# Performance work log

Measured on AMD Instinct MI355X. Metric: run time of the kernel, lower is better.

## Reference

```python
import jax, jax.numpy as jnp
import numpy as np

B, S, D_MODEL, N_HEADS, D_K, D_V = 4, 1024, 1024, 16, 64, 64
LN_EPS = 1e-5


def setup_inputs() -> dict:
    key = jax.random.key(0)
    ks = jax.random.split(key, 10)
    inp = {
        "input_Q": jax.random.normal(ks[0], (B, S, D_MODEL), dtype=jnp.float32),
        "input_K": jax.random.normal(ks[1], (B, S, D_MODEL), dtype=jnp.float32),
        "input_V": jax.random.normal(ks[2], (B, S, D_MODEL), dtype=jnp.float32),
        "attn_mask": jax.random.randint(ks[3], (B, S, S), 0, 2) > 0,
        "res_att": jax.random.normal(ks[4], (B, N_HEADS, S, S), dtype=jnp.float32),
        # weights stored as [in, out] (torch Linear applies x @ W.T)
        "W_Q": jax.random.normal(ks[5], (D_MODEL, N_HEADS * D_K), dtype=jnp.float32) * 0.02,
        "W_K": jax.random.normal(ks[6], (D_MODEL, N_HEADS * D_K), dtype=jnp.float32) * 0.02,
        "W_V": jax.random.normal(ks[7], (D_MODEL, N_HEADS * D_V), dtype=jnp.float32) * 0.02,
        "W_fc": jax.random.normal(ks[8], (N_HEADS * D_V, D_MODEL), dtype=jnp.float32) * 0.02,
        "ln_gamma": jnp.ones((D_MODEL,), dtype=jnp.float32),
        "ln_beta": jnp.zeros((D_MODEL,), dtype=jnp.float32),
    }
    return inp


def layer_norm(x, gamma, beta):
    mu = jnp.mean(x, axis=-1, keepdims=True)
    var = jnp.mean((x - mu) ** 2, axis=-1, keepdims=True)
    return (x - mu) * jax.lax.rsqrt(var + LN_EPS) * gamma + beta


def reference(input_Q, input_K, input_V, attn_mask, res_att,
              W_Q, W_K, W_V, W_fc, ln_gamma, ln_beta):
    b, s, _ = input_Q.shape
    residual = input_Q
    # project and split heads: [B, H, S, d]
    Q = (input_Q @ W_Q).reshape(b, s, N_HEADS, D_K).transpose(0, 2, 1, 3)
    K = (input_K @ W_K).reshape(b, -1, N_HEADS, D_K).transpose(0, 2, 1, 3)
    V = (input_V @ W_V).reshape(b, -1, N_HEADS, D_V).transpose(0, 2, 1, 3)
    # scores [B, H, Sq, Sk] + residual attention bias
    scores = jnp.einsum("bhqd,bhkd->bhqk", Q, K) / np.sqrt(D_K).astype(np.float32)
    scores = scores + res_att
    scores = jnp.where(attn_mask[:, None, :, :], jnp.float32(-1e9), scores)
    attn = jax.nn.softmax(scores, axis=-1)
    context = jnp.einsum("bhqk,bhkd->bhqd", attn, V)
    context = context.transpose(0, 2, 1, 3).reshape(b, s, N_HEADS * D_V)
    output = context @ W_fc
    out = layer_norm(output + residual, ln_gamma, ln_beta)
    return (out, attn)
```

## Files before the change

### kernel.cpp

```cpp
#include <hip/hip_runtime.h>
#include <hip/hip_fp16.h>


typedef short short8 __attribute__((ext_vector_type(8)));
typedef unsigned short ushort8 __attribute__((ext_vector_type(8)));
typedef float f32x4 __attribute__((ext_vector_type(4)));
typedef int i32x4 __attribute__((ext_vector_type(4)));

__device__ __forceinline__ unsigned short f2bf(float f) {
  unsigned int u = __float_as_uint(f);
  u += 0x7fffu + ((u >> 16) & 1u);
  return (unsigned short)(u >> 16);
}

#define BAR() do { asm volatile("s_waitcnt lgkmcnt(0)" ::: "memory"); \
                   __builtin_amdgcn_s_barrier(); } while (0)

__global__ __launch_bounds__(256) void cvt3_kernel(
    const float* __restrict__ a, const float* __restrict__ b, const float* __restrict__ c,
    unsigned short* __restrict__ oa, unsigned short* __restrict__ ob, unsigned short* __restrict__ oc)
{
  const float* src = blockIdx.y == 0 ? a : (blockIdx.y == 1 ? b : c);
  unsigned short* dst = blockIdx.y == 0 ? oa : (blockIdx.y == 1 ? ob : oc);
  size_t i = (size_t)blockIdx.x * 256 + threadIdx.x;
  float4 v = ((const float4*)src)[i];
  ushort4 o;
  o.x = f2bf(v.x); o.y = f2bf(v.y); o.z = f2bf(v.z); o.w = f2bf(v.w);
  ((ushort4*)dst)[i] = o;
}

__global__ void wtrans_kernel(
    const float* __restrict__ w0, const float* __restrict__ w1,
    const float* __restrict__ w2, const float* __restrict__ w3,
    unsigned short* __restrict__ o0, unsigned short* __restrict__ o1,
    unsigned short* __restrict__ o2, unsigned short* __restrict__ o3)
{
  __shared__ float tile[32][33];
  int z = blockIdx.z;
  const float* src = z == 0 ? w0 : (z == 1 ? w1 : (z == 2 ? w2 : w3));
  unsigned short* dst = z == 0 ? o0 : (z == 1 ? o1 : (z == 2 ? o2 : o3));
  int bx = blockIdx.x * 32;
  int by = blockIdx.y * 32;
  int tx = threadIdx.x, ty = threadIdx.y;
#pragma unroll
  for (int i = 0; i < 4; ++i)
    tile[ty + 8 * i][tx] = src[(size_t)(by + ty + 8 * i) * 1024 + bx + tx];
  __syncthreads();
#pragma unroll
  for (int i = 0; i < 4; ++i)
    dst[(size_t)(bx + ty + 8 * i) * 1024 + by + tx] = f2bf(tile[tx][ty + 8 * i]);
}

__device__ __forceinline__ void gemm_core(const unsigned short* __restrict__ A,
                                          const unsigned short* __restrict__ Bt,
                                          int m0, int n0, f32x4 (&acc)[4][4])
{
  __shared__ unsigned short As[128][40];
  __shared__ unsigned short Bs[128][40];
  const int tid = threadIdx.x;
  const int lane = tid & 63;
  const int w = tid >> 6;
  const int wm = (w >> 1) << 6;
  const int wn = (w & 1) << 6;
  const int lr = lane & 15;
  const int lk = (lane >> 4) << 3;

  f32x4 zero = {0.f, 0.f, 0.f, 0.f};
#pragma unroll
  for (int mi = 0; mi < 4; ++mi)
#pragma unroll
    for (int ni = 0; ni < 4; ++ni) acc[mi][ni] = zero;

  for (int kt = 0; kt < 1024; kt += 32) {
    __syncthreads();
#pragma unroll
    for (int i = 0; i < 2; ++i) {
      int c = tid + (i << 8);
      int r = c >> 2, ko = (c & 3) << 3;
      *(short8*)&As[r][ko] = *(const short8*)&A[(size_t)(m0 + r) * 1024 + kt + ko];
      *(short8*)&Bs[r][ko] = *(const short8*)&Bt[(size_t)(n0 + r) * 1024 + kt + ko];
    }
    __syncthreads();
    short8 a[4], b[4];
#pragma unroll
    for (int mi = 0; mi < 4; ++mi) a[mi] = *(const short8*)&As[wm + mi * 16 + lr][lk];
#pragma unroll
    for (int ni = 0; ni < 4; ++ni) b[ni] = *(const short8*)&Bs[wn + ni * 16 + lr][lk];
#pragma unroll
    for (int mi = 0; mi < 4; ++mi)
#pragma unroll
      for (int ni = 0; ni < 4; ++ni)
        acc[mi][ni] = __builtin_amdgcn_mfma_f32_16x16x32_bf16(a[mi], b[ni], acc[mi][ni], 0, 0, 0);
  }
}

__global__ __launch_bounds__(256) void proj_gemm(
    const unsigned short* __restrict__ Xq, const unsigned short* __restrict__ Xk,
    const unsigned short* __restrict__ Xv,
    const unsigned short* __restrict__ Wtq, const unsigned short* __restrict__ Wtk,
    const unsigned short* __restrict__ Wtv,
    unsigned short* __restrict__ Qp, unsigned short* __restrict__ Kp,
    unsigned short* __restrict__ Vpt)
{
  const int mode = blockIdx.z;
  const unsigned short* A = mode == 0 ? Xq : (mode == 1 ? Xk : Xv);
  const unsigned short* Bt = mode == 0 ? Wtq : (mode == 1 ? Wtk : Wtv);
  const int m0 = blockIdx.y * 128;
  const int n0 = blockIdx.x * 128;

  f32x4 acc[4][4];
  gemm_core(A, Bt, m0, n0, acc);

  const int lane = threadIdx.x & 63;
  const int w = threadIdx.x >> 6;
  const int wm = (w >> 1) << 6;
  const int wn = (w & 1) << 6;
  const int lr = lane & 15;
  const int lg = lane >> 4;
  const float scale = (mode == 0) ? 0.125f : 1.0f;
  unsigned short* dst01 = (mode == 0) ? Qp : Kp;

#pragma unroll
  for (int mi = 0; mi < 4; ++mi)
#pragma unroll
    for (int ni = 0; ni < 4; ++ni)
#pragma unroll
      for (int r = 0; r < 4; ++r) {
        int m = m0 + wm + mi * 16 + (lg << 2) + r;
        int n = n0 + wn + ni * 16 + lr;
        float v = acc[mi][ni][r] * scale;
        int bb = m >> 10, ss = m & 1023, hh = n >> 6, dd = n & 63;
        if (mode < 2)
          dst01[((((size_t)bb * 16 + hh) << 10) + ss) * 64 + dd] = f2bf(v);
        else
          Vpt[((((size_t)bb * 16 + hh) * 64 + dd) << 10) + ss] = f2bf(v);
      }
}

__global__ __launch_bounds__(256) void fc_gemm(
    const unsigned short* __restrict__ Ctx, const unsigned short* __restrict__ Wtf,
    float* __restrict__ OutLin)
{
  const int m0 = blockIdx.y * 128;
  const int n0 = blockIdx.x * 128;
  f32x4 acc[4][4];
  gemm_core(Ctx, Wtf, m0, n0, acc);

  const int lane = threadIdx.x & 63;
  const int w = threadIdx.x >> 6;
  const int wm = (w >> 1) << 6;
  const int wn = (w & 1) << 6;
  const int lr = lane & 15;
  const int lg = lane >> 4;
#pragma unroll
  for (int mi = 0; mi < 4; ++mi)
#pragma unroll
    for (int ni = 0; ni < 4; ++ni)
#pragma unroll
      for (int r = 0; r < 4; ++r) {
        int m = m0 + wm + mi * 16 + (lg << 2) + r;
        int n = n0 + wn + ni * 16 + lr;
        OutLin[(size_t)m * 1024 + n] = acc[mi][ni][r];
      }
}

__global__ __launch_bounds__(256) void attn_kernel(
    const unsigned short* __restrict__ Qp, const unsigned short* __restrict__ Kp,
    const unsigned short* __restrict__ Vpt,
    const float* __restrict__ res_att, const int* __restrict__ mask,
    float* __restrict__ attn_out, unsigned short* __restrict__ Ctx)
{
  __shared__ unsigned short S16[16 * 1024];
  const int qb = blockIdx.x, h = blockIdx.y, b = blockIdx.z;
  const int q0 = qb * 16;
  const int tid = threadIdx.x;
  const int lane = tid & 63;
  const int w = tid >> 6;
  const int lr = lane & 15;
  const int lg = lane >> 4;
  const int lk = lg << 3;

  const unsigned short* Qbh = Qp + (((size_t)b * 16 + h) << 16);
  const unsigned short* Kbh = Kp + (((size_t)b * 16 + h) << 16);
  const unsigned short* Vbh = Vpt + (((size_t)b * 16 + h) << 16);
  const float* res_row = res_att + ((((size_t)b * 16 + h) * 1024 + q0) << 10);
  const int* msk_row = mask + ((((size_t)b) * 1024 + q0) << 10);
  float* attn_row = attn_out + ((((size_t)b * 16 + h) * 1024 + q0) << 10);

  short8 aq0 = *(const short8*)&Qbh[(size_t)(q0 + lr) * 64 + lk];
  short8 aq1 = *(const short8*)&Qbh[(size_t)(q0 + lr) * 64 + 32 + lk];

  f32x4 zero = {0.f, 0.f, 0.f, 0.f};
#pragma unroll 2
  for (int t = 0; t < 16; ++t) {
    int n0 = (w * 16 + t) * 16;
    short8 bk0 = *(const short8*)&Kbh[(size_t)(n0 + lr) * 64 + lk];
    short8 bk1 = *(const short8*)&Kbh[(size_t)(n0 + lr) * 64 + 32 + lk];
    int col = n0 + lr;
    float rr0 = __builtin_nontemporal_load(&res_row[((size_t)(lg * 4 + 0) << 10) + col]);
    float rr1 = __builtin_nontemporal_load(&res_row[((size_t)(lg * 4 + 1) << 10) + col]);
    float rr2 = __builtin_nontemporal_load(&res_row[((size_t)(lg * 4 + 2) << 10) + col]);
    float rr3 = __builtin_nontemporal_load(&res_row[((size_t)(lg * 4 + 3) << 10) + col]);
    int mm0 = msk_row[((size_t)(lg * 4 + 0) << 10) + col];
    int mm1 = msk_row[((size_t)(lg * 4 + 1) << 10) + col];
    int mm2 = msk_row[((size_t)(lg * 4 + 2) << 10) + col];
    int mm3 = msk_row[((size_t)(lg * 4 + 3) << 10) + col];
    f32x4 acc = zero;
    acc = __builtin_amdgcn_mfma_f32_16x16x32_bf16(aq0, bk0, acc, 0, 0, 0);
    acc = __builtin_amdgcn_mfma_f32_16x16x32_bf16(aq1, bk1, acc, 0, 0, 0);
    float s0 = mm0 ? -30000.f : acc[0] + rr0;
    float s1 = mm1 ? -30000.f : acc[1] + rr1;
    float s2 = mm2 ? -30000.f : acc[2] + rr2;
    float s3 = mm3 ? -30000.f : acc[3] + rr3;
    int cbase = (((col >> 3) ^ ((lg * 4) & 7)) << 3) | (col & 7);
#pragma unroll
    for (int r = 0; r < 4; ++r) {
      int row = lg * 4 + r;
      int idx = row * 1024 + ((((col >> 3) ^ (row & 7)) << 3) | (col & 7));
      float sv = (r == 0) ? s0 : (r == 1) ? s1 : (r == 2) ? s2 : s3;
      S16[idx] = __half_as_ushort(__float2half(sv));
    }
    (void)cbase;
  }

  BAR();

#pragma unroll
  for (int j = 0; j < 4; ++j) {
    const int r_ = w + 4 * j;
    const int swz_ = r_ & 7;
    ushort8 hv0 = *(const ushort8*)&S16[r_ * 1024 + ((lane ^ swz_) << 3)];
    ushort8 hv1 = *(const ushort8*)&S16[r_ * 1024 + (((64 + lane) ^ swz_) << 3)];
    float sv[16];
#pragma unroll
    for (int e = 0; e < 8; ++e) {
      sv[e]     = __expf(__half2float(__ushort_as_half(hv0[e])));
      sv[8 + e] = __expf(__half2float(__ushort_as_half(hv1[e])));
    }
    float s01 = sv[0] + sv[1], s23 = sv[2] + sv[3];
    float s45 = sv[4] + sv[5], s67 = sv[6] + sv[7];
    float s89 = sv[8] + sv[9], sab = sv[10] + sv[11];
    float scd = sv[12] + sv[13], sef = sv[14] + sv[15];
    float sum = ((s01 + s23) + (s45 + s67)) + ((s89 + sab) + (scd + sef));
#pragma unroll
    for (int off = 32; off >= 1; off >>= 1) sum += __shfl_xor(sum, off);
    float inv = 1.f / sum;
#pragma unroll
    for (int i = 0; i < 16; ++i) sv[i] *= inv;
    f32x4* att4 = (f32x4*)(attn_row + ((size_t)r_ << 10));
    f32x4 o0 = {sv[0], sv[1], sv[2], sv[3]};
    f32x4 o1 = {sv[4], sv[5], sv[6], sv[7]};
    f32x4 o2 = {sv[8], sv[9], sv[10], sv[11]};
    f32x4 o3 = {sv[12], sv[13], sv[14], sv[15]};
    att4[lane * 2] = o0;
    att4[lane * 2 + 1] = o1;
    att4[128 + lane * 2] = o2;
    att4[128 + lane * 2 + 1] = o3;
    ushort8 q0_, q1_;
#pragma unroll
    for (int e = 0; e < 8; ++e) { q0_[e] = f2bf(sv[e]); q1_[e] = f2bf(sv[8 + e]); }
    *(ushort8*)&S16[r_ * 1024 + ((lane ^ swz_) << 3)] = q0_;
    *(ushort8*)&S16[r_ * 1024 + (((64 + lane) ^ swz_) << 3)] = q1_;
  }

  BAR();

  f32x4 co = zero;
  const int dv0 = w * 16;
  const int pswz = lr & 7;
#pragma unroll 4
  for (int ks = 0; ks < 32; ++ks) {
    int u = (ks << 2) + lg;
    short8 pa = *(const short8*)&S16[lr * 1024 + ((u ^ pswz) << 3)];
    short8 bv = *(const short8*)&Vbh[(size_t)(dv0 + lr) * 1024 + (ks << 5) + lk];
    co = __builtin_amdgcn_mfma_f32_16x16x32_bf16(pa, bv, co, 0, 0, 0);
  }
#pragma unroll
  for (int r = 0; r < 4; ++r) {
    int row = (lg << 2) + r;
    Ctx[((size_t)(b * 1024 + q0 + row)) * 1024 + h * 64 + dv0 + lr] = f2bf(co[r]);
  }
}

__global__ __launch_bounds__(256) void ln_kernel(
    const float* __restrict__ xlin, const float* __restrict__ resid,
    const float* __restrict__ gamma, const float* __restrict__ beta,
    float* __restrict__ out)
{
  const int m = blockIdx.x;
  const int t = threadIdx.x;
  float4 v = ((const float4*)(xlin + ((size_t)m << 10)))[t];
  float4 rq = ((const float4*)(resid + ((size_t)m << 10)))[t];
  v.x += rq.x; v.y += rq.y; v.z += rq.z; v.w += rq.w;
  float s = v.x + v.y + v.z + v.w;
  float s2 = v.x * v.x + v.y * v.y + v.z * v.z + v.w * v.w;
#pragma unroll
  for (int off = 32; off >= 1; off >>= 1) {
    s += __shfl_xor(s, off);
    s2 += __shfl_xor(s2, off);
  }
  __shared__ float rs[4], rs2[4];
  const int w = t >> 6, lane = t & 63;
  if (lane == 0) { rs[w] = s; rs2[w] = s2; }
  __syncthreads();
  s = rs[0] + rs[1] + rs[2] + rs[3];
  s2 = rs2[0] + rs2[1] + rs2[2] + rs2[3];
  float mu = s * (1.f / 1024.f);
  float var = s2 * (1.f / 1024.f) - mu * mu;
  float rstd = rsqrtf(var + 1e-5f);
  float4 g = ((const float4*)gamma)[t];
  float4 bt = ((const float4*)beta)[t];
  float4 o;
  o.x = (v.x - mu) * rstd * g.x + bt.x;
  o.y = (v.y - mu) * rstd * g.y + bt.y;
  o.z = (v.z - mu) * rstd * g.z + bt.z;
  o.w = (v.w - mu) * rstd * g.w + bt.w;
  ((float4*)(out + ((size_t)m << 10)))[t] = o;
}

extern "C" void kernel_launch(void* const* d_in, const int* in_sizes, int n_in,
                              void* d_out, int out_size, void* d_ws, size_t ws_size,
                              hipStream_t stream) {
  const float* inQ = (const float*)d_in[0];
  const float* inK = (const float*)d_in[1];
  const float* inV = (const float*)d_in[2];
  const int* msk = (const int*)d_in[3];
  const float* res = (const float*)d_in[4];
  const float* wq = (const float*)d_in[5];
  const float* wk = (const float*)d_in[6];
  const float* wv = (const float*)d_in[7];
  const float* wfc = (const float*)d_in[8];
  const float* gamma = (const float*)d_in[9];
  const float* beta = (const float*)d_in[10];

  unsigned short* Xq = (unsigned short*)d_ws;
  unsigned short* Xk = Xq + 4194304;
  unsigned short* Xv = Xk + 4194304;
  unsigned short* Wtq = Xv + 4194304;
  unsigned short* Wtk = Wtq + 1048576;
  unsigned short* Wtv = Wtk + 1048576;
  unsigned short* Wtf = Wtv + 1048576;
  unsigned short* Qp = Wtf + 1048576;
  unsigned short* Kp = Qp + 4194304;
  unsigned short* Vpt = Kp + 4194304;
  unsigned short* Ctx = Vpt + 4194304;
  float* OutLin = (float*)d_ws;

  float* out = (float*)d_out;
  float* attn_out = out + 4194304;

  cvt3_kernel<<<dim3(4096, 3, 1), 256, 0, stream>>>(inQ, inK, inV, Xq, Xk, Xv);
  wtrans_kernel<<<dim3(32, 32, 4), dim3(32, 8, 1), 0, stream>>>(wq, wk, wv, wfc, Wtq, Wtk, Wtv, Wtf);
  proj_gemm<<<dim3(8, 32, 3), 256, 0, stream>>>(Xq, Xk, Xv, Wtq, Wtk, Wtv, Qp, Kp, Vpt);
  attn_kernel<<<dim3(64, 16, 4), 256, 0, stream>>>(Qp, Kp, Vpt, res, msk, attn_out, Ctx);
  fc_gemm<<<dim3(8, 32, 1), 256, 0, stream>>>(Ctx, Wtf, OutLin);
  ln_kernel<<<dim3(4096, 1, 1), 256, 0, stream>>>(OutLin, inQ, gamma, beta, out);
}
```

Before: 319.6 us.

## Compute exp in score pass, defer softmax normalization to attn write and PV output

The score loop now applies exp directly and accumulates per-row partial sums in registers, reducing them across lanes and waves through a small shared array. Unnormalized exp values are stored as bf16 in LDS and used unnormalized for the PV matmul, with the 1/sum scaling applied to the context output instead. This removes the second LDS write pass, one barrier, and the per-row wave reductions. In exchange, attn values are now derived from bf16-rounded exponentials rather than fp16 scores, there is no max subtraction so exp can overflow on large scores, and masked entries become exact zeros.

Result: slower. 339.1 us (+6.1%).

```diff
diff --git a/kernel.cpp b/kernel.cpp
--- a/kernel.cpp
+++ b/kernel.cpp
@@ -11,6 +11,9 @@
   unsigned int u = __float_as_uint(f);
   u += 0x7fffu + ((u >> 16) & 1u);
   return (unsigned short)(u >> 16);
+}
+__device__ __forceinline__ float bf2f(unsigned short u) {
+  return __uint_as_float(((unsigned int)u) << 16);
 }
 
 #define BAR() do { asm volatile("s_waitcnt lgkmcnt(0)" ::: "memory"); \
@@ -171,6 +174,7 @@
     float* __restrict__ attn_out, unsigned short* __restrict__ Ctx)
 {
   __shared__ unsigned short S16[16 * 1024];
+  __shared__ float part[4][4][4];
   const int qb = blockIdx.x, h = blockIdx.y, b = blockIdx.z;
   const int q0 = qb * 16;
   const int tid = threadIdx.x;
@@ -191,6 +195,7 @@
   short8 aq1 = *(const short8*)&Qbh[(size_t)(q0 + lr) * 64 + 32 + lk];
 
   f32x4 zero = {0.f, 0.f, 0.f, 0.f};
+  float psum0 = 0.f, psum1 = 0.f, psum2 = 0.f, psum3 = 0.f;
 #pragma unroll 2
   for (int t = 0; t < 16; ++t) {
     int n0 = (w * 16 + t) * 16;
@@ -208,19 +213,33 @@
     f32x4 acc = zero;
     acc = __builtin_amdgcn_mfma_f32_16x16x32_bf16(aq0, bk0, acc, 0, 0, 0);
     acc = __builtin_amdgcn_mfma_f32_16x16x32_bf16(aq1, bk1, acc, 0, 0, 0);
-    float s0 = mm0 ? -30000.f : acc[0] + rr0;
-    float s1 = mm1 ? -30000.f : acc[1] + rr1;
-    float s2 = mm2 ? -30000.f : acc[2] + rr2;
-    float s3 = mm3 ? -30000.f : acc[3] + rr3;
-    int cbase = (((col >> 3) ^ ((lg * 4) & 7)) << 3) | (col & 7);
+    float e0 = mm0 ? 0.f : __expf(acc[0] + rr0);
+    float e1 = mm1 ? 0.f : __expf(acc[1] + rr1);
+    float e2 = mm2 ? 0.f : __expf(acc[2] + rr2);
+    float e3 = mm3 ? 0.f : __expf(acc[3] + rr3);
+    psum0 += e0; psum1 += e1; psum2 += e2; psum3 += e3;
+    int cs = ((((col >> 3)) << 3) | (col & 7));
 #pragma unroll
     for (int r = 0; r < 4; ++r) {
       int row = lg * 4 + r;
       int idx = row * 1024 + ((((col >> 3) ^ (row & 7)) << 3) | (col & 7));
-      float sv = (r == 0) ? s0 : (r == 1) ? s1 : (r == 2) ? s2 : s3;
-      S16[idx] = __half_as_ushort(__float2half(sv));
+      float ev = (r == 0) ? e0 : (r == 1) ? e1 : (r == 2) ? e2 : e3;
+      S16[idx] = f2bf(ev);
     }
-    (void)cbase;
+    (void)cs;
+  }
+#pragma unroll
+  for (int off = 1; off <= 8; off <<= 1) {
+    psum0 += __shfl_xor(psum0, off);
+    psum1 += __shfl_xor(psum1, off);
+    psum2 += __shfl_xor(psum2, off);
+    psum3 += __shfl_xor(psum3, off);
+  }
+  if (lr == 0) {
+    part[w][lg][0] = psum0;
+    part[w][lg][1] = psum1;
+    part[w][lg][2] = psum2;
+    part[w][lg][3] = psum3;
   }
 
   BAR();
@@ -229,41 +248,25 @@
   for (int j = 0; j < 4; ++j) {
     const int r_ = w + 4 * j;
     const int swz_ = r_ & 7;
+    const int lgr = r_ >> 2, rr_ = r_ & 3;
+    float sum = part[0][lgr][rr_] + part[1][lgr][rr_] + part[2][lgr][rr_] + part[3][lgr][rr_];
+    float inv = 1.f / sum;
     ushort8 hv0 = *(const ushort8*)&S16[r_ * 1024 + ((lane ^ swz_) << 3)];
     ushort8 hv1 = *(const ushort8*)&S16[r_ * 1024 + (((64 + lane) ^ swz_) << 3)];
-    float sv[16];
-#pragma unroll
-    for (int e = 0; e < 8; ++e) {
-      sv[e]     = __expf(__half2float(__ushort_as_half(hv0[e])));
-      sv[8 + e] = __expf(__half2float(__ushort_as_half(hv1[e])));
+    f32x4 o0, o1, o2, o3;
+#pragma unroll
+    for (int e = 0; e < 4; ++e) {
+      o0[e] = bf2f(hv0[e]) * inv;
+      o1[e] = bf2f(hv0[4 + e]) * inv;
+      o2[e] = bf2f(hv1[e]) * inv;
+      o3[e] = bf2f(hv1[4 + e]) * inv;
     }
-    float s01 = sv[0] + sv[1], s23 = sv[2] + sv[3];
-    float s45 = sv[4] + sv[5], s67 = sv[6] + sv[7];
-    float s89 = sv[8] + sv[9], sab = sv[10] + sv[11];
-    float scd = sv[12] + sv[13], sef = sv[14] + sv[15];
-    float sum = ((s01 + s23) + (s45 + s67)) + ((s89 + sab) + (scd + sef));
-#pragma unroll
-    for (int off = 32; off >= 1; off >>= 1) sum += __shfl_xor(sum, off);
-    float inv = 1.f / sum;
-#pragma unroll
-    for (int i = 0; i < 16; ++i) sv[i] *= inv;
     f32x4* att4 = (f32x4*)(attn_row + ((size_t)r_ << 10));
-    f32x4 o0 = {sv[0], sv[1], sv[2], sv[3]};
-    f32x4 o1 = {sv[4], sv[5], sv[6], sv[7]};
-    f32x4 o2 = {sv[8], sv[9], sv[10], sv[11]};
-    f32x4 o3 = {sv[12], sv[13], sv[14], sv[15]};
     att4[lane * 2] = o0;
     att4[lane * 2 + 1] = o1;
     att4[128 + lane * 2] = o2;
     att4[128 + lane * 2 + 1] = o3;
-    ushort8 q0_, q1_;
-#pragma unroll
-    for (int e = 0; e < 8; ++e) { q0_[e] = f2bf(sv[e]); q1_[e] = f2bf(sv[8 + e]); }
-    *(ushort8*)&S16[r_ * 1024 + ((lane ^ swz_) << 3)] = q0_;
-    *(ushort8*)&S16[r_ * 1024 + (((64 + lane) ^ swz_) << 3)] = q1_;
-  }
-
-  BAR();
+  }
 
   f32x4 co = zero;
   const int dv0 = w * 16;
@@ -278,7 +281,9 @@
 #pragma unroll
   for (int r = 0; r < 4; ++r) {
     int row = (lg << 2) + r;
-    Ctx[((size_t)(b * 1024 + q0 + row)) * 1024 + h * 64 + dv0 + lr] = f2bf(co[r]);
+    float sum = part[0][lg][r] + part[1][lg][r] + part[2][lg][r] + part[3][lg][r];
+    float inv = 1.f / sum;
+    Ctx[((size_t)(b * 1024 + q0 + row)) * 1024 + h * 64 + dv0 + lr] = f2bf(co[r] * inv);
   }
 }
 
```

## Split attention into QK-exp kernel and PV-normalize kernel via bf16 scratch

Applied to the files above, without the earlier changes.

Replaces the single fused attention kernel with two kernels. The first computes QK scores, adds the residual bias, applies the mask and exp, writes unnormalized bf16 exponentials to a 128MB workspace, and stores per-wave partial row sums. The second reads those exponentials to write the normalized fp32 attention and to run the PV MFMA product. The intent is to remove the LDS staging and barrier of the fused kernel and raise occupancy, at the cost of an extra large global round trip for the exponentials. It also drops the max subtraction, so exp can overflow if scores are large, and falls back to the fused kernel when the workspace is too small.

Result: slower. 479.2 us (+49.9%).

```diff
diff --git a/kernel.cpp b/kernel.cpp
--- a/kernel.cpp
+++ b/kernel.cpp
@@ -11,6 +11,9 @@
   unsigned int u = __float_as_uint(f);
   u += 0x7fffu + ((u >> 16) & 1u);
   return (unsigned short)(u >> 16);
+}
+__device__ __forceinline__ float bf2f(unsigned short u) {
+  return __uint_as_float(((unsigned int)u) << 16);
 }
 
 #define BAR() do { asm volatile("s_waitcnt lgkmcnt(0)" ::: "memory"); \
@@ -164,7 +167,138 @@
       }
 }
 
-__global__ __launch_bounds__(256) void attn_kernel(
+
+__global__ __launch_bounds__(256) void qk_exp_kernel(
+    const unsigned short* __restrict__ Qp, const unsigned short* __restrict__ Kp,
+    const float* __restrict__ res_att, const int* __restrict__ mask,
+    unsigned short* __restrict__ E, float* __restrict__ psum_ws)
+{
+  const int qb = blockIdx.x, h = blockIdx.y, b = blockIdx.z;
+  const int bh = b * 16 + h;
+  const int q0 = qb * 16;
+  const int tid = threadIdx.x;
+  const int lane = tid & 63;
+  const int w = tid >> 6;
+  const int lr = lane & 15;
+  const int lg = lane >> 4;
+  const int lk = lg << 3;
+
+  const unsigned short* Qbh = Qp + ((size_t)bh << 16);
+  const unsigned short* Kbh = Kp + ((size_t)bh << 16);
+  const float* res_row = res_att + (((size_t)bh * 1024 + q0) << 10);
+  const int* msk_row = mask + ((((size_t)b) * 1024 + q0) << 10);
+  unsigned short* e_row = E + (((size_t)bh * 1024 + q0) << 10);
+
+  short8 aq0 = *(const short8*)&Qbh[(size_t)(q0 + lr) * 64 + lk];
+  short8 aq1 = *(const short8*)&Qbh[(size_t)(q0 + lr) * 64 + 32 + lk];
+
+  f32x4 zero = {0.f, 0.f, 0.f, 0.f};
+  float psum0 = 0.f, psum1 = 0.f, psum2 = 0.f, psum3 = 0.f;
+#pragma unroll 2
+  for (int t = 0; t < 16; ++t) {
+    int n0 = (w * 16 + t) * 16;
+    short8 bk0 = *(const short8*)&Kbh[(size_t)(n0 + lr) * 64 + lk];
+    short8 bk1 = *(const short8*)&Kbh[(size_t)(n0 + lr) * 64 + 32 + lk];
+    int col = n0 + lr;
+    float rr0 = __builtin_nontemporal_load(&res_row[((size_t)(lg * 4 + 0) << 10) + col]);
+    float rr1 = __builtin_nontemporal_load(&res_row[((size_t)(lg * 4 + 1) << 10) + col]);
+    float rr2 = __builtin_nontemporal_load(&res_row[((size_t)(lg * 4 + 2) << 10) + col]);
+    float rr3 = __builtin_nontemporal_load(&res_row[((size_t)(lg * 4 + 3) << 10) + col]);
+    int mm0 = msk_row[((size_t)(lg * 4 + 0) << 10) + col];
+    int mm1 = msk_row[((size_t)(lg * 4 + 1) << 10) + col];
+    int mm2 = msk_row[((size_t)(lg * 4 + 2) << 10) + col];
+    int mm3 = msk_row[((size_t)(lg * 4 + 3) << 10) + col];
+    f32x4 acc = zero;
+    acc = __builtin_amdgcn_mfma_f32_16x16x32_bf16(aq0, bk0, acc, 0, 0, 0);
+    acc = __builtin_amdgcn_mfma_f32_16x16x32_bf16(aq1, bk1, acc, 0, 0, 0);
+    float e0 = mm0 ? 0.f : __expf(acc[0] + rr0);
+    float e1 = mm1 ? 0.f : __expf(acc[1] + rr1);
+    float e2 = mm2 ? 0.f : __expf(acc[2] + rr2);
+    float e3 = mm3 ? 0.f : __expf(acc[3] + rr3);
+    psum0 += e0; psum1 += e1; psum2 += e2; psum3 += e3;
+    e_row[((size_t)(lg * 4 + 0) << 10) + col] = f2bf(e0);
+    e_row[((size_t)(lg * 4 + 1) << 10) + col] = f2bf(e1);
+    e_row[((size_t)(lg * 4 + 2) << 10) + col] = f2bf(e2);
+    e_row[((size_t)(lg * 4 + 3) << 10) + col] = f2bf(e3);
+  }
+#pragma unroll
+  for (int off = 1; off <= 8; off <<= 1) {
+    psum0 += __shfl_xor(psum0, off);
+    psum1 += __shfl_xor(psum1, off);
+    psum2 += __shfl_xor(psum2, off);
+    psum3 += __shfl_xor(psum3, off);
+  }
+  if (lr == 0) {
+    size_t base = ((size_t)bh * 1024 + q0 + lg * 4) * 4 + w;
+    psum_ws[base] = psum0;
+    psum_ws[base + 4] = psum1;
+    psum_ws[base + 8] = psum2;
+    psum_ws[base + 12] = psum3;
+  }
+}
+
+__global__ __launch_bounds__(256) void pv_norm_kernel(
+    const unsigned short* __restrict__ E, const float* __restrict__ psum_ws,
+    const unsigned short* __restrict__ Vpt,
+    float* __restrict__ attn_out, unsigned short* __restrict__ Ctx)
+{
+  const int qb = blockIdx.x, h = blockIdx.y, b = blockIdx.z;
+  const int bh = b * 16 + h;
+  const int q0 = qb * 16;
+  const int tid = threadIdx.x;
+  const int lane = tid & 63;
+  const int w = tid >> 6;
+  const int lr = lane & 15;
+  const int lg = lane >> 4;
+  const int lk = lg << 3;
+
+  const unsigned short* e_base = E + (((size_t)bh * 1024 + q0) << 10);
+  const unsigned short* Vbh = Vpt + ((size_t)bh << 16);
+  float* attn_row = attn_out + (((size_t)bh * 1024 + q0) << 10);
+  const float* ps_base = psum_ws + ((size_t)bh * 1024 + q0) * 4;
+
+#pragma unroll
+  for (int j = 0; j < 4; ++j) {
+    const int r_ = w + 4 * j;
+    f32x4 ps = *(const f32x4*)&ps_base[(size_t)r_ * 4];
+    float inv = 1.f / (ps[0] + ps[1] + ps[2] + ps[3]);
+    const unsigned short* erow = e_base + ((size_t)r_ << 10);
+    ushort8 hv0 = *(const ushort8*)&erow[lane << 3];
+    ushort8 hv1 = *(const ushort8*)&erow[(64 + lane) << 3];
+    f32x4 o0, o1, o2, o3;
+#pragma unroll
+    for (int e = 0; e < 4; ++e) {
+      o0[e] = bf2f(hv0[e]) * inv;
+      o1[e] = bf2f(hv0[4 + e]) * inv;
+      o2[e] = bf2f(hv1[e]) * inv;
+      o3[e] = bf2f(hv1[4 + e]) * inv;
+    }
+    f32x4* att4 = (f32x4*)(attn_row + ((size_t)r_ << 10));
+    att4[lane * 2] = o0;
+    att4[lane * 2 + 1] = o1;
+    att4[128 + lane * 2] = o2;
+    att4[128 + lane * 2 + 1] = o3;
+  }
+
+  f32x4 zero = {0.f, 0.f, 0.f, 0.f};
+  f32x4 co = zero;
+  const int dv0 = w * 16;
+#pragma unroll 4
+  for (int ks = 0; ks < 32; ++ks) {
+    short8 pa = *(const short8*)&e_base[((size_t)lr << 10) + (ks << 5) + lk];
+    short8 bv = *(const short8*)&Vbh[(size_t)(dv0 + lr) * 1024 + (ks << 5) + lk];
+    co = __builtin_amdgcn_mfma_f32_16x16x32_bf16(pa, bv, co, 0, 0, 0);
+  }
+#pragma unroll
+  for (int r = 0; r < 4; ++r) {
+    int row = (lg << 2) + r;
+    f32x4 ps = *(const f32x4*)&ps_base[(size_t)row * 4];
+    float inv = 1.f / (ps[0] + ps[1] + ps[2] + ps[3]);
+    Ctx[((size_t)(b * 1024 + q0 + row)) * 1024 + h * 64 + dv0 + lr] = f2bf(co[r] * inv);
+  }
+}
+
+__global__ __launch_bounds__(256) void fused_attn(
     const unsigned short* __restrict__ Qp, const unsigned short* __restrict__ Kp,
     const unsigned short* __restrict__ Vpt,
     const float* __restrict__ res_att, const int* __restrict__ mask,
@@ -212,7 +346,6 @@
     float s1 = mm1 ? -30000.f : acc[1] + rr1;
     float s2 = mm2 ? -30000.f : acc[2] + rr2;
     float s3 = mm3 ? -30000.f : acc[3] + rr3;
-    int cbase = (((col >> 3) ^ ((lg * 4) & 7)) << 3) | (col & 7);
 #pragma unroll
     for (int r = 0; r < 4; ++r) {
       int row = lg * 4 + r;
@@ -220,7 +353,6 @@
       float sv = (r == 0) ? s0 : (r == 1) ? s1 : (r == 2) ? s2 : s3;
       S16[idx] = __half_as_ushort(__float2half(sv));
     }
-    (void)cbase;
   }
 
   BAR();
@@ -344,15 +476,26 @@
   unsigned short* Kp = Qp + 4194304;
   unsigned short* Vpt = Kp + 4194304;
   unsigned short* Ctx = Vpt + 4194304;
+  unsigned short* E = Ctx + 4194304;
+  float* psum_ws = (float*)(E + 67108864);
   float* OutLin = (float*)d_ws;
 
   float* out = (float*)d_out;
   float* attn_out = out + 4194304;
+
+  const size_t need = (size_t)(32 + 64 + 1) * 1024 * 1024 * 2;
 
   cvt3_kernel<<<dim3(4096, 3, 1), 256, 0, stream>>>(inQ, inK, inV, Xq, Xk, Xv);
   wtrans_kernel<<<dim3(32, 32, 4), dim3(32, 8, 1), 0, stream>>>(wq, wk, wv, wfc, Wtq, Wtk, Wtv, Wtf);
   proj_gemm<<<dim3(8, 32, 3), 256, 0, stream>>>(Xq, Xk, Xv, Wtq, Wtk, Wtv, Qp, Kp, Vpt);
-  attn_kernel<<<dim3(64, 16, 4), 256, 0, stream>>>(Qp, Kp, Vpt, res, msk, attn_out, Ctx);
+
+  if (ws_size >= need) {
+    qk_exp_kernel<<<dim3(64, 16, 4), 256, 0, stream>>>(Qp, Kp, res, msk, E, psum_ws);
+    pv_norm_kernel<<<dim3(64, 16, 4), 256, 0, stream>>>(E, psum_ws, Vpt, attn_out, Ctx);
+  } else {
+    fused_attn<<<dim3(64, 16, 4), 256, 0, stream>>>(Qp, Kp, Vpt, res, msk, attn_out, Ctx);
+  }
+
   fc_gemm<<<dim3(8, 32, 1), 256, 0, stream>>>(Ctx, Wtf, OutLin);
   ln_kernel<<<dim3(4096, 1, 1), 256, 0, stream>>>(OutLin, inQ, gamma, beta, out);
 }
```
